# Optimization experiments

Hardware: AMD Instinct MI355X
Metric: run time of the kernel (lower is better)

## Reference

```python
import jax, jax.numpy as jnp
import numpy as np

B = 4096
D = 256
TEMP = 0.5


def setup_inputs() -> dict:
    key = jax.random.key(0)
    k1, k2 = jax.random.split(key)
    x_i = jax.random.normal(k1, (B, D), dtype=jnp.float32)
    x_j = jax.random.normal(k2, (B, D), dtype=jnp.float32)
    return {"x_i": x_i, "x_j": x_j}


def reference(x_i, x_j):
    b = x_i.shape[0]
    # L2-normalize rows (F.normalize with default eps=1e-12)
    def l2norm(x):
        n = jnp.linalg.norm(x, axis=1, keepdims=True)
        return x / jnp.maximum(n, 1e-12)

    z = jnp.concatenate([l2norm(x_i), l2norm(x_j)], axis=0)  # [2B, D]
    # rows of z are unit-norm, so cosine similarity == dot product
    sim = z @ z.T  # [2B, 2B]

    # positives: diagonals at offsets +B and -B
    idx = jnp.arange(b)
    sim_ij = sim[idx, idx + b]
    sim_ji = sim[idx + b, idx]
    pos = jnp.concatenate([sim_ij, sim_ji], axis=0)  # [2B]

    nom = jnp.exp(pos / TEMP)
    neg_mask = 1.0 - jnp.eye(2 * b, dtype=sim.dtype)
    denom = jnp.sum(neg_mask * jnp.exp(sim / TEMP), axis=1)  # [2B]
    loss = jnp.sum(-jnp.log(nom / denom)) / (2 * b)
    return loss
```

## Files before the change

kernel.cpp:

```cpp
#include <hip/hip_runtime.h>

#define NB   4096
#define ND   256
#define N2B  8192
#define INV_T 2.0f
#define NBAND 64
#define NTRI  2080

typedef __attribute__((ext_vector_type(8))) short bf16x8;
typedef __attribute__((ext_vector_type(4))) float f32x4;

__device__ __forceinline__ void gload_lds16(const void* g, void* l) {
  __builtin_amdgcn_global_load_lds(
      (const __attribute__((address_space(1))) void*)g,
      (__attribute__((address_space(3))) void*)l, 16, 0, 0);
}

__device__ __forceinline__ unsigned short f2b(float f) {
  unsigned int u = __float_as_uint(f);
  u = (u + 0x7fffu + ((u >> 16) & 1u)) >> 16;
  return (unsigned short)u;
}
__device__ __forceinline__ float b2f(unsigned short h) {
  return __uint_as_float(((unsigned int)h) << 16);
}

__global__ __launch_bounds__(256) void k_normalize(
    const float* __restrict__ xi, const float* __restrict__ xj,
    unsigned short* __restrict__ Z, float* __restrict__ diagE,
    float* __restrict__ pos, float* __restrict__ lossAcc,
    unsigned int* __restrict__ ticket) {
  __shared__ float sh[2][256];
  if (blockIdx.x == 0 && threadIdx.x == 0) { *lossAcc = 0.0f; *ticket = 0u; }
  int wave = threadIdx.x >> 6, lane = threadIdx.x & 63;
  int r = (int)blockIdx.x * 2 + (wave & 1);
  bool isJ = wave >= 2;
  const float* src = (isJ ? xj : xi) + (size_t)r * ND;
  int zrow = r + (isJ ? NB : 0);

  float4 v = *(const float4*)(src + lane * 4);
  float ss = v.x * v.x + v.y * v.y + v.z * v.z + v.w * v.w;
#pragma unroll
  for (int m = 1; m < 64; m <<= 1) ss += __shfl_xor(ss, m, 64);
  float scale = 1.0f / fmaxf(sqrtf(ss), 1e-12f);
  unsigned short h0 = f2b(v.x * scale), h1 = f2b(v.y * scale);
  unsigned short h2 = f2b(v.z * scale), h3 = f2b(v.w * scale);
  ushort4 st; st.x = h0; st.y = h1; st.z = h2; st.w = h3;
  *(ushort4*)(Z + (size_t)zrow * ND + lane * 4) = st;

  float f0 = b2f(h0), f1 = b2f(h1), f2 = b2f(h2), f3 = b2f(h3);
  float d = f0 * f0 + f1 * f1 + f2 * f2 + f3 * f3;
#pragma unroll
  for (int m = 1; m < 64; m <<= 1) d += __shfl_xor(d, m, 64);
  if (lane == 0) diagE[zrow] = __expf(d * INV_T);

  if (isJ) {
    float* s = sh[wave & 1] + lane * 4;
    s[0] = f0; s[1] = f1; s[2] = f2; s[3] = f3;
  }
  __syncthreads();
  if (!isJ) {
    const float* s = sh[wave] + lane * 4;
    float p = f0 * s[0] + f1 * s[1] + f2 * s[2] + f3 * s[3];
#pragma unroll
    for (int m = 1; m < 64; m <<= 1) p += __shfl_xor(p, m, 64);
    if (lane == 0) pos[r] = p;
  }
}

__global__ __launch_bounds__(256, 2) void k_sym(
    const unsigned short* __restrict__ Z, float* __restrict__ P) {
  __shared__ alignas(16) unsigned short Bs[128 * ND];

  int tid = threadIdx.x;
  int wave = tid >> 6, lane = tid & 63;
  int quad = lane >> 4, c16 = lane & 15;

  int g = ((int)blockIdx.x & 7) * (NTRI / 8) + ((int)blockIdx.x >> 3);
  int SI = 0, SJ = 0, u = g;
  bool found = false;
  for (int si = 0; si < 8 && !found; ++si) {
    for (int sj = si; sj < 8; ++sj) {
      int sz = (si == sj) ? 36 : 64;
      if (u < sz) { SI = si; SJ = sj; found = true; break; }
      u -= sz;
    }
  }
  int ti, tj;
  if (SI == SJ) {
    ti = 0;
    while (u >= 8 - ti) { u -= 8 - ti; ++ti; }
    tj = ti + u;
  } else {
    ti = u >> 3; tj = u & 7;
  }
  int I = SI * 8 + ti, J = SJ * 8 + tj;
  bool diag = (I == J);

  int rowA = I * 128, rowB = J * 128;

  int lr1 = lane >> 5, cs = lane & 31;
#pragma unroll
  for (int j = 0; j < 16; ++j) {
    int r0 = wave * 32 + j * 2;
    int row = r0 + lr1;
    int gc = cs ^ (row & 31);
    gload_lds16(Z + (size_t)(rowB + row) * ND + gc * 8, &Bs[r0 * ND]);
  }

  bf16x8 afr[2][8];
  int wrow = rowA + wave * 32;
#pragma unroll
  for (int rg = 0; rg < 2; ++rg)
#pragma unroll
    for (int kk = 0; kk < 8; ++kk)
      afr[rg][kk] = *(const bf16x8*)(Z + (size_t)(wrow + rg * 16 + c16) * ND +
                                     kk * 32 + quad * 8);

  asm volatile("s_waitcnt vmcnt(0)" ::: "memory");
  __syncthreads();

  f32x4 acc[2][8] = {};
  __builtin_amdgcn_s_setprio(1);
#pragma unroll
  for (int kk = 0; kk < 8; ++kk) {
    bf16x8 bfr[8];
#pragma unroll
    for (int ni = 0; ni < 8; ++ni) {
      int row = ni * 16 + c16;
      int slot = (kk * 4 + quad) ^ (row & 31);
      bfr[ni] = *(const bf16x8*)&Bs[row * ND + slot * 8];
    }
#pragma unroll
    for (int rg = 0; rg < 2; ++rg)
#pragma unroll
      for (int ni = 0; ni < 8; ++ni)
        acc[rg][ni] = __builtin_amdgcn_mfma_f32_16x16x32_bf16(
            afr[rg][kk], bfr[ni], acc[rg][ni], 0, 0, 0);
  }
  __builtin_amdgcn_s_setprio(0);

  float rs[2][4];
  float csum[8];
#pragma unroll
  for (int ni = 0; ni < 8; ++ni) csum[ni] = 0.0f;
#pragma unroll
  for (int rg = 0; rg < 2; ++rg)
#pragma unroll
    for (int r = 0; r < 4; ++r) rs[rg][r] = 0.0f;

#pragma unroll
  for (int rg = 0; rg < 2; ++rg)
#pragma unroll
    for (int ni = 0; ni < 8; ++ni)
#pragma unroll
      for (int r = 0; r < 4; ++r) {
        float e = __expf(acc[rg][ni][r] * INV_T);
        rs[rg][r] += e;
        csum[ni] += e;
      }

#pragma unroll
  for (int m = 1; m <= 8; m <<= 1)
#pragma unroll
    for (int rg = 0; rg < 2; ++rg)
#pragma unroll
      for (int r = 0; r < 4; ++r)
        rs[rg][r] += __shfl_xor(rs[rg][r], m, 64);

#pragma unroll
  for (int rg = 0; rg < 2; ++rg)
#pragma unroll
    for (int r = 0; r < 4; ++r)
      if (c16 == rg * 4 + r) {
        int row = wrow + rg * 16 + quad * 4 + r;
        P[(size_t)row * NBAND + J] = rs[rg][r];
      }

  if (!diag) {
#pragma unroll
    for (int ni = 0; ni < 8; ++ni) {
      csum[ni] += __shfl_xor(csum[ni], 16, 64);
      csum[ni] += __shfl_xor(csum[ni], 32, 64);
    }
    __syncthreads();
    float* colred = (float*)Bs;
    if (lane < 16) {
#pragma unroll
      for (int ni = 0; ni < 8; ++ni)
        colred[wave * 128 + ni * 16 + lane] = csum[ni];
    }
    __syncthreads();
    if (tid < 128) {
      float v = colred[tid] + colred[128 + tid] + colred[256 + tid] +
                colred[384 + tid];
      P[(size_t)(rowB + tid) * NBAND + I] = v;
    }
  }
}

__global__ __launch_bounds__(256) void k_final(
    const float* __restrict__ P, const float* __restrict__ diagE,
    const float* __restrict__ pos, float* __restrict__ lossAcc,
    unsigned int* __restrict__ ticket, float* __restrict__ out) {
  __shared__ float red[4];
  int tid = threadIdx.x;
  int wave = tid >> 6, lane = tid & 63;
  int row = (int)blockIdx.x * 256 + tid;

  const float4* Pr = (const float4*)(P + (size_t)row * NBAND);
  float s = 0.0f;
#pragma unroll
  for (int q = 0; q < 16; ++q) {
    float4 a = Pr[q];
    s += (a.x + a.y) + (a.z + a.w);
  }
  s -= diagE[row];
  float term = __logf(s) - INV_T * pos[row & (NB - 1)];
#pragma unroll
  for (int m = 1; m < 64; m <<= 1) term += __shfl_xor(term, m, 64);
  if (lane == 0) red[wave] = term;
  __syncthreads();
  if (tid == 0) {
    float bs = red[0] + red[1] + red[2] + red[3];
    atomicAdd(lossAcc, bs);
    __threadfence();
    unsigned int old = atomicAdd(ticket, 1u);
    if (old == 31u) {
      float v = atomicAdd(lossAcc, 0.0f);
      out[0] = v * (1.0f / (float)N2B);
    }
  }
}

extern "C" void kernel_launch(void* const* d_in, const int* in_sizes, int n_in,
                              void* d_out, int out_size, void* d_ws,
                              size_t ws_size, hipStream_t stream) {
  const float* xi = (const float*)d_in[0];
  const float* xj = (const float*)d_in[1];
  float* out = (float*)d_out;
  char* ws = (char*)d_ws;
  unsigned short* Z = (unsigned short*)ws;
  float* P = (float*)(ws + (4u << 20));
  float* pos = (float*)(ws + (6u << 20));
  float* diagE = (float*)(ws + (6u << 20) + 65536);
  float* lossAcc = (float*)(ws + (6u << 20) + 131072);
  unsigned int* ticket = (unsigned int*)(ws + (6u << 20) + 131072 + 64);

  k_normalize<<<dim3(NB / 2), dim3(256), 0, stream>>>(xi, xj, Z, diagE, pos,
                                                      lossAcc, ticket);
  k_sym<<<dim3(NTRI), dim3(256), 0, stream>>>(Z, P);
  k_final<<<dim3(32), dim3(256), 0, stream>>>(P, diagE, pos, lossAcc, ticket,
                                              out);
}
```

Measured before the change: 108.4 us.

## Double-buffer B tile in 32-column chunks and use DPP row reductions

The k_sym kernel now streams the 128-row B tile in four 32-row chunks through a double-buffered LDS area, prefetching the next chunk while the current one runs through MFMA and exp. This cuts LDS use from 64KB to about 33KB and lowers the accumulator register count, which could raise occupancy and overlap load latency with compute. Column sums are reduced and written per chunk. Row sums now use DPP row-shift adds instead of shfl_xor. The cost is an extra barrier and vmcnt wait per chunk.

```diff
diff --git a/kernel.cpp b/kernel.cpp
--- a/kernel.cpp
+++ b/kernel.cpp
@@ -5,7 +5,7 @@
 #define N2B  8192
 #define INV_T 2.0f
 #define NBAND 64
-#define NTRI  2080
+#define NTILE 2080
 
 typedef __attribute__((ext_vector_type(8))) short bf16x8;
 typedef __attribute__((ext_vector_type(4))) float f32x4;
@@ -23,6 +23,19 @@
 }
 __device__ __forceinline__ float b2f(unsigned short h) {
   return __uint_as_float(((unsigned int)h) << 16);
+}
+
+__device__ __forceinline__ float row_sum16(float v) {
+  int x;
+  x = __builtin_amdgcn_update_dpp(0, __float_as_int(v), 0x128, 0xF, 0xF, 0);
+  v += __int_as_float(x);
+  x = __builtin_amdgcn_update_dpp(0, __float_as_int(v), 0x124, 0xF, 0xF, 0);
+  v += __int_as_float(x);
+  x = __builtin_amdgcn_update_dpp(0, __float_as_int(v), 0x122, 0xF, 0xF, 0);
+  v += __int_as_float(x);
+  x = __builtin_amdgcn_update_dpp(0, __float_as_int(v), 0x121, 0xF, 0xF, 0);
+  v += __int_as_float(x);
+  return v;
 }
 
 __global__ __launch_bounds__(256) void k_normalize(
@@ -70,19 +83,21 @@
 
 __global__ __launch_bounds__(256, 2) void k_sym(
     const unsigned short* __restrict__ Z, float* __restrict__ P) {
-  __shared__ alignas(16) unsigned short Bs[128 * ND];
+  __shared__ alignas(16) unsigned short Bsh[2][32 * ND];
+  __shared__ float colred[2][4][32];
 
   int tid = threadIdx.x;
   int wave = tid >> 6, lane = tid & 63;
   int quad = lane >> 4, c16 = lane & 15;
-
-  int g = ((int)blockIdx.x & 7) * (NTRI / 8) + ((int)blockIdx.x >> 3);
+  int lr1 = lane >> 5, cs = lane & 31;
+
+  int g = ((int)blockIdx.x & 7) * (NTILE / 8) + ((int)blockIdx.x >> 3);
   int SI = 0, SJ = 0, u = g;
   bool found = false;
-  for (int si = 0; si < 8 && !found; ++si) {
-    for (int sj = si; sj < 8; ++sj) {
-      int sz = (si == sj) ? 36 : 64;
-      if (u < sz) { SI = si; SJ = sj; found = true; break; }
+  for (int a = 0; a < 8 && !found; ++a) {
+    for (int b = a; b < 8; ++b) {
+      int sz = (a == b) ? 36 : 64;
+      if (u < sz) { SI = a; SJ = b; found = true; break; }
       u -= sz;
     }
   }
@@ -97,16 +112,7 @@
   int I = SI * 8 + ti, J = SJ * 8 + tj;
   bool diag = (I == J);
 
-  int rowA = I * 128, rowB = J * 128;
-
-  int lr1 = lane >> 5, cs = lane & 31;
-#pragma unroll
-  for (int j = 0; j < 16; ++j) {
-    int r0 = wave * 32 + j * 2;
-    int row = r0 + lr1;
-    int gc = cs ^ (row & 31);
-    gload_lds16(Z + (size_t)(rowB + row) * ND + gc * 8, &Bs[r0 * ND]);
-  }
+  int rowA = I * 128, colB0 = J * 128;
 
   bf16x8 afr[2][8];
   int wrow = rowA + wave * 32;
@@ -117,56 +123,87 @@
       afr[rg][kk] = *(const bf16x8*)(Z + (size_t)(wrow + rg * 16 + c16) * ND +
                                      kk * 32 + quad * 8);
 
+  auto STAGE = [&](int c, int h) {
+    int base = colB0 + c * 32;
+#pragma unroll
+    for (int j = 0; j < 4; ++j) {
+      int r0 = wave * 8 + j * 2;
+      int row = r0 + lr1;
+      int gc = cs ^ row;
+      gload_lds16(Z + (size_t)(base + row) * ND + gc * 8, &Bsh[h][r0 * ND]);
+    }
+  };
+
+  STAGE(0, 0);
   asm volatile("s_waitcnt vmcnt(0)" ::: "memory");
   __syncthreads();
 
-  f32x4 acc[2][8] = {};
-  __builtin_amdgcn_s_setprio(1);
-#pragma unroll
-  for (int kk = 0; kk < 8; ++kk) {
-    bf16x8 bfr[8];
-#pragma unroll
-    for (int ni = 0; ni < 8; ++ni) {
-      int row = ni * 16 + c16;
-      int slot = (kk * 4 + quad) ^ (row & 31);
-      bfr[ni] = *(const bf16x8*)&Bs[row * ND + slot * 8];
-    }
+  float rs[2][4];
+#pragma unroll
+  for (int rg = 0; rg < 2; ++rg)
+#pragma unroll
+    for (int r = 0; r < 4; ++r) rs[rg][r] = 0.0f;
+
+  for (int c = 0; c < 4; ++c) {
+    int h = c & 1;
+    if (c + 1 < 4) STAGE(c + 1, h ^ 1);
+
+    f32x4 acc[2][2] = {};
+    __builtin_amdgcn_s_setprio(1);
+#pragma unroll
+    for (int kk = 0; kk < 8; ++kk) {
+      bf16x8 bfr[2];
+#pragma unroll
+      for (int ni = 0; ni < 2; ++ni) {
+        int row = ni * 16 + c16;
+        int slot = (kk * 4 + quad) ^ row;
+        bfr[ni] = *(const bf16x8*)&Bsh[h][row * ND + slot * 8];
+      }
+#pragma unroll
+      for (int rg = 0; rg < 2; ++rg)
+#pragma unroll
+        for (int ni = 0; ni < 2; ++ni)
+          acc[rg][ni] = __builtin_amdgcn_mfma_f32_16x16x32_bf16(
+              afr[rg][kk], bfr[ni], acc[rg][ni], 0, 0, 0);
+    }
+    __builtin_amdgcn_s_setprio(0);
+
+    float csum[2] = {0.0f, 0.0f};
 #pragma unroll
     for (int rg = 0; rg < 2; ++rg)
 #pragma unroll
-      for (int ni = 0; ni < 8; ++ni)
-        acc[rg][ni] = __builtin_amdgcn_mfma_f32_16x16x32_bf16(
-            afr[rg][kk], bfr[ni], acc[rg][ni], 0, 0, 0);
-  }
-  __builtin_amdgcn_s_setprio(0);
-
-  float rs[2][4];
-  float csum[8];
-#pragma unroll
-  for (int ni = 0; ni < 8; ++ni) csum[ni] = 0.0f;
-#pragma unroll
-  for (int rg = 0; rg < 2; ++rg)
-#pragma unroll
-    for (int r = 0; r < 4; ++r) rs[rg][r] = 0.0f;
-
-#pragma unroll
-  for (int rg = 0; rg < 2; ++rg)
-#pragma unroll
-    for (int ni = 0; ni < 8; ++ni)
-#pragma unroll
-      for (int r = 0; r < 4; ++r) {
-        float e = __expf(acc[rg][ni][r] * INV_T);
-        rs[rg][r] += e;
-        csum[ni] += e;
-      }
-
-#pragma unroll
-  for (int m = 1; m <= 8; m <<= 1)
-#pragma unroll
-    for (int rg = 0; rg < 2; ++rg)
-#pragma unroll
-      for (int r = 0; r < 4; ++r)
-        rs[rg][r] += __shfl_xor(rs[rg][r], m, 64);
+      for (int ni = 0; ni < 2; ++ni)
+#pragma unroll
+        for (int r = 0; r < 4; ++r) {
+          float e = __expf(acc[rg][ni][r] * INV_T);
+          rs[rg][r] += e;
+          csum[ni] += e;
+        }
+
+#pragma unroll
+    for (int ni = 0; ni < 2; ++ni) {
+      csum[ni] += __shfl_xor(csum[ni], 16, 64);
+      csum[ni] += __shfl_xor(csum[ni], 32, 64);
+    }
+    if (lane < 16) {
+      colred[h][wave][lane] = csum[0];
+      colred[h][wave][16 + lane] = csum[1];
+    }
+
+    asm volatile("s_waitcnt vmcnt(0)" ::: "memory");
+    __syncthreads();
+
+    if (!diag && tid < 32) {
+      float v = colred[h][0][tid] + colred[h][1][tid] + colred[h][2][tid] +
+                colred[h][3][tid];
+      P[(size_t)(colB0 + c * 32 + tid) * NBAND + I] = v;
+    }
+  }
+
+#pragma unroll
+  for (int rg = 0; rg < 2; ++rg)
+#pragma unroll
+    for (int r = 0; r < 4; ++r) rs[rg][r] = row_sum16(rs[rg][r]);
 
 #pragma unroll
   for (int rg = 0; rg < 2; ++rg)
@@ -176,27 +213,6 @@
         int row = wrow + rg * 16 + quad * 4 + r;
         P[(size_t)row * NBAND + J] = rs[rg][r];
       }
-
-  if (!diag) {
-#pragma unroll
-    for (int ni = 0; ni < 8; ++ni) {
-      csum[ni] += __shfl_xor(csum[ni], 16, 64);
-      csum[ni] += __shfl_xor(csum[ni], 32, 64);
-    }
-    __syncthreads();
-    float* colred = (float*)Bs;
-    if (lane < 16) {
-#pragma unroll
-      for (int ni = 0; ni < 8; ++ni)
-        colred[wave * 128 + ni * 16 + lane] = csum[ni];
-    }
-    __syncthreads();
-    if (tid < 128) {
-      float v = colred[tid] + colred[128 + tid] + colred[256 + tid] +
-                colred[384 + tid];
-      P[(size_t)(rowB + tid) * NBAND + I] = v;
-    }
-  }
 }
 
 __global__ __launch_bounds__(256) void k_final(
@@ -249,7 +265,7 @@
 
   k_normalize<<<dim3(NB / 2), dim3(256), 0, stream>>>(xi, xj, Z, diagE, pos,
                                                       lossAcc, ticket);
-  k_sym<<<dim3(NTRI), dim3(256), 0, stream>>>(Z, P);
+  k_sym<<<dim3(NTILE), dim3(256), 0, stream>>>(Z, P);
   k_final<<<dim3(32), dim3(256), 0, stream>>>(P, diagE, pos, lossAcc, ticket,
                                               out);
 }
```

After: 103.8 us. -4.3%, faster.
